# Kernel optimization log

Hardware: AMD Instinct MI355X
Metric: run time of the kernel (lower is better)

## Reference

```python
import jax, jax.numpy as jnp
import numpy as np

N_NODES = 150000
N_EDGES = 2400000
F_IN, HID, N_CLS = 22, 32, 6
BN_EPS = 1e-5


def setup_inputs() -> dict:
    key = jax.random.key(0)
    ks = jax.random.split(key, 10)
    x = jax.random.normal(ks[0], (N_NODES, F_IN), dtype=jnp.float32)
    edge_index = jax.random.randint(ks[1], (2, N_EDGES), 0, N_NODES, dtype=jnp.int64)
    # xavier-uniform style linear weights, zero biases (as in _init_weights)
    def xavier(k, fan_in, fan_out):
        lim = float(np.sqrt(6.0 / (fan_in + fan_out)))
        return jax.random.uniform(k, (fan_in, fan_out), jnp.float32, -lim, lim)
    return {
        "x": x,
        "edge_index": edge_index,
        "W_emb": xavier(ks[2], F_IN, HID),
        "b_emb": jnp.zeros((HID,), jnp.float32),
        "W_gcn": xavier(ks[3], HID, HID),
        "b_gcn": jnp.zeros((HID,), jnp.float32),
        "gamma": jnp.ones((HID,), jnp.float32),
        "beta": jnp.zeros((HID,), jnp.float32),
        "W_cls": xavier(ks[4], HID, N_CLS),
        "b_cls": jnp.zeros((N_CLS,), jnp.float32),
    }


def reference(x, edge_index, W_emb, b_emb, W_gcn, b_gcn, gamma, beta, W_cls, b_cls):
    N = x.shape[0]
    # embedding + relu
    h = jax.nn.relu(x @ W_emb + b_emb)                      # [N, HID]
    # GCNConv: linear transform first
    h = h @ W_gcn                                           # [N, HID]
    # add self-loops
    loops = jnp.arange(N, dtype=edge_index.dtype)
    src = jnp.concatenate([edge_index[0], loops])           # [E+N]
    dst = jnp.concatenate([edge_index[1], loops])
    # symmetric normalization deg^{-1/2} A_hat deg^{-1/2}
    deg = jax.ops.segment_sum(jnp.ones_like(dst, dtype=h.dtype), dst, num_segments=N)
    dis = jnp.where(deg > 0, jax.lax.rsqrt(jnp.where(deg > 0, deg, 1.0)), 0.0)
    norm = dis[src] * dis[dst]                              # [E+N]
    msg = h[src] * norm[:, None]                            # gather + scale
    agg = jax.ops.segment_sum(msg, dst, num_segments=N) + b_gcn
    # BatchNorm1d (training-mode batch statistics, biased variance)
    mean = jnp.mean(agg, axis=0)
    var = jnp.mean((agg - mean) ** 2, axis=0)
    hn = (agg - mean) * jax.lax.rsqrt(var + BN_EPS) * gamma + beta
    hn = jax.nn.relu(hn)
    # dropout is identity in eval; classifier
    return hn @ W_cls + b_cls
```

## Files before the change

### kernel.cpp

```cpp
#include <hip/hip_runtime.h>

#define N_NODES 150000
#define N_EDGES 2400000
#define F_IN    22
#define HID     32
#define N_CLS   6
#define BN_EPS  1e-5f

#define BSHIFT  8
#define BMASK   255
#define NB      ((N_NODES + BMASK) >> BSHIFT)
#define CHUNK   8192
#define NBLK_BIN ((N_EDGES + CHUNK - 1) / CHUNK)
#define CHUNK_H 8192
#define NBLK_H  ((N_EDGES + CHUNK_H - 1) / CHUNK_H)
#define NBLK_EMB ((N_NODES + 255) / 256)
#define NREP    8

__global__ void embed_hist_kernel(const float* __restrict__ x,
                                  const float* __restrict__ W_emb,
                                  const float* __restrict__ b_emb,
                                  const float* __restrict__ W_gcn,
                                  float* __restrict__ h,
                                  const int* __restrict__ dst,
                                  int* __restrict__ bcnt) {
    if (blockIdx.x < NBLK_EMB) {
        __shared__ float sWe[F_IN * HID];
        __shared__ float sbe[HID];
        __shared__ float sWg[HID * HID];
        for (int t = threadIdx.x; t < F_IN * HID; t += blockDim.x) sWe[t] = W_emb[t];
        if (threadIdx.x < HID) sbe[threadIdx.x] = b_emb[threadIdx.x];
        for (int t = threadIdx.x; t < HID * HID; t += blockDim.x) sWg[t] = W_gcn[t];
        __syncthreads();

        int i = blockIdx.x * blockDim.x + threadIdx.x;
        if (i >= N_NODES) return;

        float xi[F_IN];
#pragma unroll
        for (int f = 0; f < F_IN; ++f) xi[f] = x[(size_t)i * F_IN + f];

        float h1[HID];
#pragma unroll
        for (int j = 0; j < HID; ++j) {
            float acc = sbe[j];
#pragma unroll
            for (int f = 0; f < F_IN; ++f) acc = fmaf(xi[f], sWe[f * HID + j], acc);
            h1[j] = fmaxf(acc, 0.0f);
        }
#pragma unroll
        for (int j = 0; j < HID; ++j) {
            float acc = 0.0f;
#pragma unroll
            for (int f = 0; f < HID; ++f) acc = fmaf(h1[f], sWg[f * HID + j], acc);
            h[(size_t)i * HID + j] = acc;
        }
    } else {
        __shared__ int hloc[NB];
        for (int t = threadIdx.x; t < NB; t += 256) hloc[t] = 0;
        __syncthreads();
        int base = (blockIdx.x - NBLK_EMB) * CHUNK_H;
        int end = base + CHUNK_H; if (end > N_EDGES) end = N_EDGES;
        for (int i = base + threadIdx.x; i < end; i += 256)
            atomicAdd(&hloc[dst[i] >> BSHIFT], 1);
        __syncthreads();
        for (int t = threadIdx.x; t < NB; t += 256)
            if (hloc[t]) atomicAdd(&bcnt[t], hloc[t]);
    }
}

__global__ void bucket_scan_kernel(const int* __restrict__ bcnt,
                                   int* __restrict__ boff,
                                   int* __restrict__ bcur) {
    __shared__ int s[1024];
    int t = threadIdx.x;
    int v0 = (t < NB) ? bcnt[t] : 0;
    s[t] = v0;
    __syncthreads();
#pragma unroll
    for (int o = 1; o < 1024; o <<= 1) {
        int v = (t >= o) ? s[t - o] : 0;
        __syncthreads();
        s[t] += v;
        __syncthreads();
    }
    if (t < NB) {
        int e = s[t] - v0;
        boff[t] = e;
        bcur[t] = e;
    }
    if (t == NB - 1) boff[NB] = s[t];
}

__global__ void bin_edges_kernel(const int* __restrict__ src,
                                 const int* __restrict__ dst,
                                 int* __restrict__ bcur,
                                 unsigned int* __restrict__ binned) {
    __shared__ int hloc[NB];
    __shared__ int base[NB];
    __shared__ int lcur[NB];
    for (int t = threadIdx.x; t < NB; t += 512) hloc[t] = 0;
    __syncthreads();

    int cbase = blockIdx.x * CHUNK;
    int cend = cbase + CHUNK; if (cend > N_EDGES) cend = N_EDGES;
    for (int i = cbase + threadIdx.x; i < cend; i += 512)
        atomicAdd(&hloc[dst[i] >> BSHIFT], 1);
    __syncthreads();
    for (int t = threadIdx.x; t < NB; t += 512) {
        int c = hloc[t];
        base[t] = c ? atomicAdd(&bcur[t], c) : 0;
        lcur[t] = 0;
    }
    __syncthreads();
    for (int i = cbase + threadIdx.x; i < cend; i += 512) {
        int d = dst[i];
        int b = d >> BSHIFT;
        int r = atomicAdd(&lcur[b], 1);
        binned[base[b] + r] = ((unsigned)(d & BMASK) << 24) | (unsigned)src[i];
    }
}

__global__ void bucket_csr_kernel(const int* __restrict__ boff,
                                  const unsigned int* __restrict__ binned,
                                  int* __restrict__ sorted_src,
                                  int* __restrict__ off,
                                  float* __restrict__ dis) {
    __shared__ int s_cnt[256];
    __shared__ int s_scan[256];
    __shared__ int s_cur[256];
    int b = blockIdx.x;
    int t = threadIdx.x;
    int s0 = boff[b], s1 = boff[b + 1];
    int nbase = b << BSHIFT;
    int nnode = N_NODES - nbase; if (nnode > 256) nnode = 256;

    s_cnt[t] = 0;
    __syncthreads();
    for (int k = s0 + t; k < s1; k += 256)
        atomicAdd(&s_cnt[binned[k] >> 24], 1);
    __syncthreads();

    int v = s_cnt[t];
    s_scan[t] = v;
    __syncthreads();
#pragma unroll
    for (int o = 1; o < 256; o <<= 1) {
        int u = (t >= o) ? s_scan[t - o] : 0;
        __syncthreads();
        s_scan[t] += u;
        __syncthreads();
    }
    int excl = s_scan[t] - v;
    s_cur[t] = excl;
    if (t < nnode) {
        off[nbase + t] = s0 + excl;
        dis[nbase + t] = rsqrtf(1.0f + (float)v);
    }
    if (b == NB - 1 && t == 0) off[N_NODES] = N_EDGES;
    __syncthreads();

    for (int k = s0 + t; k < s1; k += 256) {
        unsigned p = binned[k];
        int n = (int)(p >> 24);
        int r = atomicAdd(&s_cur[n], 1);
        sorted_src[s0 + r] = (int)(p & 0xFFFFFFu);
    }
}

__global__ void aggregate_kernel(const int* __restrict__ off,
                                 const int* __restrict__ sorted_src,
                                 const float* __restrict__ h,
                                 const float* __restrict__ dis,
                                 float* __restrict__ agg,
                                 float* __restrict__ stats) {
    int t = blockIdx.x * blockDim.x + threadIdx.x;
    int node = t >> 3;
    int c = t & 7;
    bool active = node < N_NODES;

    float4 ps = {0.f, 0.f, 0.f, 0.f};
    float4 pq = {0.f, 0.f, 0.f, 0.f};

    if (active) {
        const float4* hrow = reinterpret_cast<const float4*>(h);
        float dn = dis[node];
        float4 hv = hrow[(size_t)node * 8 + c];
        float4 a0, a1, a2, a3;
        a0.x = hv.x * dn; a0.y = hv.y * dn; a0.z = hv.z * dn; a0.w = hv.w * dn;
        a1 = a2 = a3 = make_float4(0.f, 0.f, 0.f, 0.f);

        int b = off[node], e = off[node + 1];
        int k = b;
        for (; k + 4 <= e; k += 4) {
            int s0 = sorted_src[k], s1 = sorted_src[k + 1];
            int s2 = sorted_src[k + 2], s3 = sorted_src[k + 3];
            float d0 = dis[s0], d1 = dis[s1], d2 = dis[s2], d3 = dis[s3];
            float4 v0 = hrow[(size_t)s0 * 8 + c];
            float4 v1 = hrow[(size_t)s1 * 8 + c];
            float4 v2 = hrow[(size_t)s2 * 8 + c];
            float4 v3 = hrow[(size_t)s3 * 8 + c];
            a0.x = fmaf(v0.x, d0, a0.x); a0.y = fmaf(v0.y, d0, a0.y);
            a0.z = fmaf(v0.z, d0, a0.z); a0.w = fmaf(v0.w, d0, a0.w);
            a1.x = fmaf(v1.x, d1, a1.x); a1.y = fmaf(v1.y, d1, a1.y);
            a1.z = fmaf(v1.z, d1, a1.z); a1.w = fmaf(v1.w, d1, a1.w);
            a2.x = fmaf(v2.x, d2, a2.x); a2.y = fmaf(v2.y, d2, a2.y);
            a2.z = fmaf(v2.z, d2, a2.z); a2.w = fmaf(v2.w, d2, a2.w);
            a3.x = fmaf(v3.x, d3, a3.x); a3.y = fmaf(v3.y, d3, a3.y);
            a3.z = fmaf(v3.z, d3, a3.z); a3.w = fmaf(v3.w, d3, a3.w);
        }
        for (; k < e; ++k) {
            int s = sorted_src[k];
            float d = dis[s];
            float4 v = hrow[(size_t)s * 8 + c];
            a0.x = fmaf(v.x, d, a0.x); a0.y = fmaf(v.y, d, a0.y);
            a0.z = fmaf(v.z, d, a0.z); a0.w = fmaf(v.w, d, a0.w);
        }
        float4 o;
        o.x = (a0.x + a1.x + a2.x + a3.x) * dn;
        o.y = (a0.y + a1.y + a2.y + a3.y) * dn;
        o.z = (a0.z + a1.z + a2.z + a3.z) * dn;
        o.w = (a0.w + a1.w + a2.w + a3.w) * dn;
        reinterpret_cast<float4*>(agg)[(size_t)node * 8 + c] = o;
        ps = o;
        pq.x = o.x * o.x; pq.y = o.y * o.y; pq.z = o.z * o.z; pq.w = o.w * o.w;
    }

    __shared__ float S[256 * 4];
    __shared__ float Q[256 * 4];
    S[threadIdx.x * 4 + 0] = ps.x; S[threadIdx.x * 4 + 1] = ps.y;
    S[threadIdx.x * 4 + 2] = ps.z; S[threadIdx.x * 4 + 3] = ps.w;
    Q[threadIdx.x * 4 + 0] = pq.x; Q[threadIdx.x * 4 + 1] = pq.y;
    Q[threadIdx.x * 4 + 2] = pq.z; Q[threadIdx.x * 4 + 3] = pq.w;
    __syncthreads();
    if (threadIdx.x < 32) {
        int cc = threadIdx.x >> 2, j = threadIdx.x & 3;
        float s = 0.0f, q = 0.0f;
#pragma unroll
        for (int w = 0; w < 32; ++w) {
            int tid = (w << 3) | cc;
            s += S[tid * 4 + j];
            q += Q[tid * 4 + j];
        }
        float* rep = stats + 64 * (blockIdx.x & (NREP - 1));
        atomicAdd(&rep[threadIdx.x], s);
        atomicAdd(&rep[32 + threadIdx.x], q);
    }
}

__global__ void cls_kernel(const float* __restrict__ agg,
                           const float* __restrict__ stats,
                           const float* __restrict__ gamma,
                           const float* __restrict__ beta,
                           const float* __restrict__ W_cls,
                           const float* __restrict__ b_cls,
                           float* __restrict__ out) {
    __shared__ float sA[HID];
    __shared__ float sB[HID];
    __shared__ float sW[HID * N_CLS];
    __shared__ float sb[N_CLS];
    if (threadIdx.x < HID) {
        float sum = 0.0f, sq = 0.0f;
#pragma unroll
        for (int r = 0; r < NREP; ++r) {
            sum += stats[r * 64 + threadIdx.x];
            sq  += stats[r * 64 + 32 + threadIdx.x];
        }
        const float invN = 1.0f / (float)N_NODES;
        float mean = sum * invN;
        float var = sq * invN - mean * mean;
        float inv = rsqrtf(var + BN_EPS);
        float A = gamma[threadIdx.x] * inv;
        sA[threadIdx.x] = A;
        sB[threadIdx.x] = beta[threadIdx.x] - mean * A;
    }
    for (int t = threadIdx.x; t < HID * N_CLS; t += blockDim.x) sW[t] = W_cls[t];
    if (threadIdx.x < N_CLS) sb[threadIdx.x] = b_cls[threadIdx.x];
    __syncthreads();

    int i = blockIdx.x * blockDim.x + threadIdx.x;
    if (i >= N_NODES) return;

    float acc[N_CLS];
#pragma unroll
    for (int c = 0; c < N_CLS; ++c) acc[c] = sb[c];
#pragma unroll
    for (int f = 0; f < HID; ++f) {
        float t = fmaxf(fmaf(agg[(size_t)i * HID + f], sA[f], sB[f]), 0.0f);
#pragma unroll
        for (int c = 0; c < N_CLS; ++c) acc[c] = fmaf(t, sW[f * N_CLS + c], acc[c]);
    }
#pragma unroll
    for (int c = 0; c < N_CLS; ++c) out[(size_t)i * N_CLS + c] = acc[c];
}

extern "C" void kernel_launch(void* const* d_in, const int* in_sizes, int n_in,
                              void* d_out, int out_size, void* d_ws, size_t ws_size,
                              hipStream_t stream) {
    const float* x     = (const float*)d_in[0];
    const int*   edge  = (const int*)d_in[1];
    const float* W_emb = (const float*)d_in[2];
    const float* b_emb = (const float*)d_in[3];
    const float* W_gcn = (const float*)d_in[4];
    const float* gamma = (const float*)d_in[6];
    const float* beta  = (const float*)d_in[7];
    const float* W_cls = (const float*)d_in[8];
    const float* b_cls = (const float*)d_in[9];
    float* out = (float*)d_out;

    float*        h          = (float*)d_ws;
    float*        agg        = h + (size_t)N_NODES * HID;
    float*        dis        = agg + (size_t)N_NODES * HID;
    int*          off        = (int*)(dis + N_NODES);
    int*          bcnt       = off + N_NODES + 1;
    int*          boff       = bcnt + NB;
    int*          bcur       = boff + NB + 1;
    unsigned int* binned     = (unsigned int*)(bcur + NB);
    int*          sorted_src = (int*)(binned + N_EDGES);
    float*        stats      = (float*)(sorted_src + N_EDGES);

    hipMemsetAsync(bcnt, 0, NB * sizeof(int), stream);
    hipMemsetAsync(stats, 0, 64 * NREP * sizeof(float), stream);

    const int* src = edge;
    const int* dst = edge + N_EDGES;

    embed_hist_kernel<<<NBLK_EMB + NBLK_H, 256, 0, stream>>>(x, W_emb, b_emb, W_gcn,
                                                             h, dst, bcnt);
    bucket_scan_kernel<<<1, 1024, 0, stream>>>(bcnt, boff, bcur);
    bin_edges_kernel<<<NBLK_BIN, 512, 0, stream>>>(src, dst, bcur, binned);
    bucket_csr_kernel<<<NB, 256, 0, stream>>>(boff, binned, sorted_src, off, dis);
    aggregate_kernel<<<(N_NODES * 8 + 255) / 256, 256, 0, stream>>>(off, sorted_src,
                                                                    h, dis, agg, stats);
    cls_kernel<<<(N_NODES + 255) / 256, 256, 0, stream>>>(agg, stats, gamma, beta,
                                                          W_cls, b_cls, out);
}
```

Before: 151.8 us.

## Store transformed node features as bf16 and widen aggregation unroll

The transformed features h are stored as packed bf16 pairs instead of fp32. This halves the bytes moved by the random per-edge gathers in the aggregation kernel. The gather loop is unrolled to eight edges per iteration so more loads are in flight. The edge-binning grid is also fixed at 256 blocks with larger chunks. The cost is reduced precision of h, which may push results outside tolerance.

```diff
diff --git a/kernel.cpp b/kernel.cpp
--- a/kernel.cpp
+++ b/kernel.cpp
@@ -10,18 +10,25 @@
 #define BSHIFT  8
 #define BMASK   255
 #define NB      ((N_NODES + BMASK) >> BSHIFT)
-#define CHUNK   8192
-#define NBLK_BIN ((N_EDGES + CHUNK - 1) / CHUNK)
+#define NBLK_BIN 256
+#define CHUNK   ((N_EDGES + NBLK_BIN - 1) / NBLK_BIN)
 #define CHUNK_H 8192
 #define NBLK_H  ((N_EDGES + CHUNK_H - 1) / CHUNK_H)
 #define NBLK_EMB ((N_NODES + 255) / 256)
 #define NREP    8
 
+__device__ __forceinline__ unsigned bf16rne(float f) {
+    unsigned u = __float_as_uint(f);
+    return (u + 0x7FFFu + ((u >> 16) & 1u)) >> 16;
+}
+__device__ __forceinline__ float bflo(unsigned p) { return __uint_as_float(p << 16); }
+__device__ __forceinline__ float bfhi(unsigned p) { return __uint_as_float(p & 0xFFFF0000u); }
+
 __global__ void embed_hist_kernel(const float* __restrict__ x,
                                   const float* __restrict__ W_emb,
                                   const float* __restrict__ b_emb,
                                   const float* __restrict__ W_gcn,
-                                  float* __restrict__ h,
+                                  unsigned* __restrict__ hb,
                                   const int* __restrict__ dst,
                                   int* __restrict__ bcnt) {
     if (blockIdx.x < NBLK_EMB) {
@@ -49,11 +56,14 @@
             h1[j] = fmaxf(acc, 0.0f);
         }
 #pragma unroll
-        for (int j = 0; j < HID; ++j) {
-            float acc = 0.0f;
-#pragma unroll
-            for (int f = 0; f < HID; ++f) acc = fmaf(h1[f], sWg[f * HID + j], acc);
-            h[(size_t)i * HID + j] = acc;
+        for (int jj = 0; jj < HID / 2; ++jj) {
+            float a0 = 0.0f, a1 = 0.0f;
+#pragma unroll
+            for (int f = 0; f < HID; ++f) {
+                a0 = fmaf(h1[f], sWg[f * HID + 2 * jj], a0);
+                a1 = fmaf(h1[f], sWg[f * HID + 2 * jj + 1], a1);
+            }
+            hb[(size_t)i * 16 + jj] = bf16rne(a0) | (bf16rne(a1) << 16);
         }
     } else {
         __shared__ int hloc[NB];
@@ -170,7 +180,7 @@
 
 __global__ void aggregate_kernel(const int* __restrict__ off,
                                  const int* __restrict__ sorted_src,
-                                 const float* __restrict__ h,
+                                 const unsigned* __restrict__ hb,
                                  const float* __restrict__ dis,
                                  float* __restrict__ agg,
                                  float* __restrict__ stats) {
@@ -183,38 +193,54 @@
     float4 pq = {0.f, 0.f, 0.f, 0.f};
 
     if (active) {
-        const float4* hrow = reinterpret_cast<const float4*>(h);
+        const uint2* hrow = reinterpret_cast<const uint2*>(hb);
         float dn = dis[node];
-        float4 hv = hrow[(size_t)node * 8 + c];
+        uint2 hp = hrow[(size_t)node * 8 + c];
         float4 a0, a1, a2, a3;
-        a0.x = hv.x * dn; a0.y = hv.y * dn; a0.z = hv.z * dn; a0.w = hv.w * dn;
+        a0.x = bflo(hp.x) * dn; a0.y = bfhi(hp.x) * dn;
+        a0.z = bflo(hp.y) * dn; a0.w = bfhi(hp.y) * dn;
         a1 = a2 = a3 = make_float4(0.f, 0.f, 0.f, 0.f);
 
         int b = off[node], e = off[node + 1];
         int k = b;
-        for (; k + 4 <= e; k += 4) {
-            int s0 = sorted_src[k], s1 = sorted_src[k + 1];
+        for (; k + 8 <= e; k += 8) {
+            int s0 = sorted_src[k],     s1 = sorted_src[k + 1];
             int s2 = sorted_src[k + 2], s3 = sorted_src[k + 3];
+            int s4 = sorted_src[k + 4], s5 = sorted_src[k + 5];
+            int s6 = sorted_src[k + 6], s7 = sorted_src[k + 7];
             float d0 = dis[s0], d1 = dis[s1], d2 = dis[s2], d3 = dis[s3];
-            float4 v0 = hrow[(size_t)s0 * 8 + c];
-            float4 v1 = hrow[(size_t)s1 * 8 + c];
-            float4 v2 = hrow[(size_t)s2 * 8 + c];
-            float4 v3 = hrow[(size_t)s3 * 8 + c];
-            a0.x = fmaf(v0.x, d0, a0.x); a0.y = fmaf(v0.y, d0, a0.y);
-            a0.z = fmaf(v0.z, d0, a0.z); a0.w = fmaf(v0.w, d0, a0.w);
-            a1.x = fmaf(v1.x, d1, a1.x); a1.y = fmaf(v1.y, d1, a1.y);
-            a1.z = fmaf(v1.z, d1, a1.z); a1.w = fmaf(v1.w, d1, a1.w);
-            a2.x = fmaf(v2.x, d2, a2.x); a2.y = fmaf(v2.y, d2, a2.y);
-            a2.z = fmaf(v2.z, d2, a2.z); a2.w = fmaf(v2.w, d2, a2.w);
-            a3.x = fmaf(v3.x, d3, a3.x); a3.y = fmaf(v3.y, d3, a3.y);
-            a3.z = fmaf(v3.z, d3, a3.z); a3.w = fmaf(v3.w, d3, a3.w);
+            float d4 = dis[s4], d5 = dis[s5], d6 = dis[s6], d7 = dis[s7];
+            uint2 v0 = hrow[(size_t)s0 * 8 + c];
+            uint2 v1 = hrow[(size_t)s1 * 8 + c];
+            uint2 v2 = hrow[(size_t)s2 * 8 + c];
+            uint2 v3 = hrow[(size_t)s3 * 8 + c];
+            uint2 v4 = hrow[(size_t)s4 * 8 + c];
+            uint2 v5 = hrow[(size_t)s5 * 8 + c];
+            uint2 v6 = hrow[(size_t)s6 * 8 + c];
+            uint2 v7 = hrow[(size_t)s7 * 8 + c];
+            a0.x = fmaf(bflo(v0.x), d0, a0.x); a0.y = fmaf(bfhi(v0.x), d0, a0.y);
+            a0.z = fmaf(bflo(v0.y), d0, a0.z); a0.w = fmaf(bfhi(v0.y), d0, a0.w);
+            a1.x = fmaf(bflo(v1.x), d1, a1.x); a1.y = fmaf(bfhi(v1.x), d1, a1.y);
+            a1.z = fmaf(bflo(v1.y), d1, a1.z); a1.w = fmaf(bfhi(v1.y), d1, a1.w);
+            a2.x = fmaf(bflo(v2.x), d2, a2.x); a2.y = fmaf(bfhi(v2.x), d2, a2.y);
+            a2.z = fmaf(bflo(v2.y), d2, a2.z); a2.w = fmaf(bfhi(v2.y), d2, a2.w);
+            a3.x = fmaf(bflo(v3.x), d3, a3.x); a3.y = fmaf(bfhi(v3.x), d3, a3.y);
+            a3.z = fmaf(bflo(v3.y), d3, a3.z); a3.w = fmaf(bfhi(v3.y), d3, a3.w);
+            a0.x = fmaf(bflo(v4.x), d4, a0.x); a0.y = fmaf(bfhi(v4.x), d4, a0.y);
+            a0.z = fmaf(bflo(v4.y), d4, a0.z); a0.w = fmaf(bfhi(v4.y), d4, a0.w);
+            a1.x = fmaf(bflo(v5.x), d5, a1.x); a1.y = fmaf(bfhi(v5.x), d5, a1.y);
+            a1.z = fmaf(bflo(v5.y), d5, a1.z); a1.w = fmaf(bfhi(v5.y), d5, a1.w);
+            a2.x = fmaf(bflo(v6.x), d6, a2.x); a2.y = fmaf(bfhi(v6.x), d6, a2.y);
+            a2.z = fmaf(bflo(v6.y), d6, a2.z); a2.w = fmaf(bfhi(v6.y), d6, a2.w);
+            a3.x = fmaf(bflo(v7.x), d7, a3.x); a3.y = fmaf(bfhi(v7.x), d7, a3.y);
+            a3.z = fmaf(bflo(v7.y), d7, a3.z); a3.w = fmaf(bfhi(v7.y), d7, a3.w);
         }
         for (; k < e; ++k) {
             int s = sorted_src[k];
             float d = dis[s];
-            float4 v = hrow[(size_t)s * 8 + c];
-            a0.x = fmaf(v.x, d, a0.x); a0.y = fmaf(v.y, d, a0.y);
-            a0.z = fmaf(v.z, d, a0.z); a0.w = fmaf(v.w, d, a0.w);
+            uint2 v = hrow[(size_t)s * 8 + c];
+            a0.x = fmaf(bflo(v.x), d, a0.x); a0.y = fmaf(bfhi(v.x), d, a0.y);
+            a0.z = fmaf(bflo(v.y), d, a0.z); a0.w = fmaf(bfhi(v.y), d, a0.w);
         }
         float4 o;
         o.x = (a0.x + a1.x + a2.x + a3.x) * dn;
@@ -308,8 +334,8 @@
     const float* b_cls = (const float*)d_in[9];
     float* out = (float*)d_out;
 
-    float*        h          = (float*)d_ws;
-    float*        agg        = h + (size_t)N_NODES * HID;
+    unsigned*     hb         = (unsigned*)d_ws;
+    float*        agg        = (float*)(hb + (size_t)N_NODES * HID / 2);
     float*        dis        = agg + (size_t)N_NODES * HID;
     int*          off        = (int*)(dis + N_NODES);
     int*          bcnt       = off + N_NODES + 1;
@@ -326,12 +352,12 @@
     const int* dst = edge + N_EDGES;
 
     embed_hist_kernel<<<NBLK_EMB + NBLK_H, 256, 0, stream>>>(x, W_emb, b_emb, W_gcn,
-                                                             h, dst, bcnt);
+                                                             hb, dst, bcnt);
     bucket_scan_kernel<<<1, 1024, 0, stream>>>(bcnt, boff, bcur);
     bin_edges_kernel<<<NBLK_BIN, 512, 0, stream>>>(src, dst, bcur, binned);
     bucket_csr_kernel<<<NB, 256, 0, stream>>>(boff, binned, sorted_src, off, dis);
     aggregate_kernel<<<(N_NODES * 8 + 255) / 256, 256, 0, stream>>>(off, sorted_src,
-                                                                    h, dis, agg, stats);
+                                                                    hb, dis, agg, stats);
     cls_kernel<<<(N_NODES + 255) / 256, 256, 0, stream>>>(agg, stats, gamma, beta,
                                                           W_cls, b_cls, out);
 }
```

Result: slower. 222.4 us (+46.6%).
